# Kernel optimization log

Hardware: AMD Instinct MI355X
Metric: run time of the kernel (lower is better)

The kernel has to match this reference:

```python
import jax, jax.numpy as jnp
import numpy as np

N, D, H, DH, DFF, E = 4096, 512, 8, 64, 2048, 65536


def setup_inputs() -> dict:
    key = jax.random.key(0)
    ks = jax.random.split(key, 20)
    g = lambda k, s: jax.random.normal(k, s, dtype=jnp.float32) * 0.02
    inp = {
        'x': jax.random.normal(ks[0], (N, D), dtype=jnp.float32),
        'edge_index': jax.random.randint(ks[1], (2, E), 0, N),
        'edge_attr': jax.random.uniform(ks[2], (E,), dtype=jnp.float32),
        'Wg': g(ks[3], (D, D)), 'bg': jnp.zeros((D,), jnp.float32),
        'ln1_s': jnp.ones((D,), jnp.float32), 'ln1_b': jnp.zeros((D,), jnp.float32),
        'Wq': g(ks[4], (D, D)), 'bq': jnp.zeros((D,), jnp.float32),
        'Wk': g(ks[5], (D, D)), 'bk': jnp.zeros((D,), jnp.float32),
        'Wv': g(ks[6], (D, D)), 'bv': jnp.zeros((D,), jnp.float32),
        'Wo': g(ks[7], (D, D)), 'bo': jnp.zeros((D,), jnp.float32),
        'ln2_s': jnp.ones((D,), jnp.float32), 'ln2_b': jnp.zeros((D,), jnp.float32),
        'W1': g(ks[8], (D, DFF)), 'b1': jnp.zeros((DFF,), jnp.float32),
        'W2': g(ks[9], (DFF, D)), 'b2': jnp.zeros((D,), jnp.float32),
        'Wa': g(ks[10], (2 * D, D)), 'ba': jnp.zeros((D,), jnp.float32),
    }
    return inp


def _ln(x, s, b):
    m = x.mean(-1, keepdims=True)
    v = ((x - m) ** 2).mean(-1, keepdims=True)
    return (x - m) * jax.lax.rsqrt(v + 1e-5) * s + b


def _gcn(x, edge_index, ew, Wg, bg):
    # GCNConv: linear, add self-loops (weight 1), sym deg normalization, scatter-add
    xt = x @ Wg                                   # [N, D]
    src = jnp.concatenate([edge_index[0], jnp.arange(N)])
    dst = jnp.concatenate([edge_index[1], jnp.arange(N)])
    w = jnp.concatenate([ew, jnp.ones((N,), ew.dtype)])
    deg = jax.ops.segment_sum(w, dst, num_segments=N)
    dinv = jnp.where(deg > 0, jax.lax.rsqrt(jnp.maximum(deg, 1e-12)), 0.0)
    coef = dinv[src] * w * dinv[dst]              # [E+N]
    out = jax.ops.segment_sum(xt[src] * coef[:, None], dst, num_segments=N)
    return out + bg


def _tfm(x, p):
    # pre-LN vanilla transformer block over all N nodes as one sequence
    h = _ln(x, p['ln1_s'], p['ln1_b'])
    q = (h @ p['Wq'] + p['bq']).reshape(N, H, DH)
    k = (h @ p['Wk'] + p['bk']).reshape(N, H, DH)
    v = (h @ p['Wv'] + p['bv']).reshape(N, H, DH)
    scores = jnp.einsum('nhd,mhd->hnm', q, k) / np.sqrt(DH)
    a = jax.nn.softmax(scores, axis=-1)
    o = jnp.einsum('hnm,mhd->nhd', a, v).reshape(N, D)
    x = x + o @ p['Wo'] + p['bo']
    h2 = _ln(x, p['ln2_s'], p['ln2_b'])
    mlp = jax.nn.gelu(h2 @ p['W1'] + p['b1']) @ p['W2'] + p['b2']
    return x + mlp


def reference(x, edge_index, edge_attr, Wg, bg, ln1_s, ln1_b, Wq, bq, Wk, bk, Wv, bv,
              Wo, bo, ln2_s, ln2_b, W1, b1, W2, b2, Wa, ba):
    p = dict(ln1_s=ln1_s, ln1_b=ln1_b, Wq=Wq, bq=bq, Wk=Wk, bk=bk, Wv=Wv, bv=bv,
             Wo=Wo, bo=bo, ln2_s=ln2_s, ln2_b=ln2_b, W1=W1, b1=b1, W2=W2, b2=b2)
    mp = _gcn(x, edge_index, edge_attr, Wg, bg)
    tf = _tfm(x, p)
    return x + jnp.concatenate([mp, tf], axis=-1) @ Wa + ba
```

## Files before the change

### kernel.cpp

```cpp
#include <hip/hip_runtime.h>
#include <math.h>

#define N_NODES 4096
#define DMODEL  512
#define NHEAD   8
#define DHEAD   64
#define DFF     2048
#define NEDGE   65536
#define QKVLD   1536

typedef unsigned short u16;
typedef __bf16 bf16x8 __attribute__((ext_vector_type(8)));
typedef float  f32x4  __attribute__((ext_vector_type(4)));
typedef short  s16x4  __attribute__((ext_vector_type(4)));

#if defined(__has_builtin)
#if __has_builtin(__builtin_amdgcn_mfma_f32_16x16x16bf16_1k)
#define HAS_MFMA_1K 1
#endif
#endif

__device__ inline f32x4 mfma16(bf16x8 a, bf16x8 b, f32x4 c) {
    return __builtin_amdgcn_mfma_f32_16x16x32_bf16(a, b, c, 0, 0, 0);
}

#ifdef HAS_MFMA_1K
__device__ inline f32x4 mfma1k(s16x4 a, s16x4 b, f32x4 c) {
    return __builtin_amdgcn_mfma_f32_16x16x16bf16_1k(a, b, c, 0, 0, 0);
}
__device__ inline s16x4 pack_bf4(f32x4 p) {
    union { float f; unsigned u; } a0, a1, a2, a3;
    a0.f = p[0]; a1.f = p[1]; a2.f = p[2]; a3.f = p[3];
    unsigned lo = __builtin_amdgcn_perm(a1.u + 0x8000u, a0.u + 0x8000u, 0x07060302u);
    unsigned hi = __builtin_amdgcn_perm(a3.u + 0x8000u, a2.u + 0x8000u, 0x07060302u);
    union { unsigned u[2]; s16x4 v; } r;
    r.u[0] = lo; r.u[1] = hi;
    return r.v;
}
#endif

__device__ inline u16 f2bf(float f) {
    union { float f; unsigned u; } v; v.f = f;
    unsigned r = v.u + 0x7fff + ((v.u >> 16) & 1);
    return (u16)(r >> 16);
}

__device__ inline float bf2f(u16 v) {
    union { unsigned u; float f; } t; t.u = ((unsigned)v) << 16; return t.f;
}

__device__ inline float gelu_tanh(float x) {
    float x3 = x * x * x;
    float t = tanhf(0.7978845608028654f * (x + 0.044715f * x3));
    return 0.5f * x * (1.0f + t);
}

#define GBN 128
#define GBK 32
#define GP  40

template <int ACT, int OBF16>
__launch_bounds__(512)
__global__ void mfma_gemm64(const u16* __restrict__ A, const u16* __restrict__ Bt,
                            const float* __restrict__ bias, const float* __restrict__ res,
                            void* __restrict__ Cout, int M, int Nn, int K, float scale,
                            int ldC, int ldRes) {
    __shared__ u16 Asm[2][64 * GP];
    __shared__ u16 Bsm[2][128 * GP];

    const int tid = threadIdx.x;
    const int w = tid >> 6;
    const int lane = tid & 63;
    const int quad = lane >> 4;
    const int l15 = lane & 15;
    const int row0 = blockIdx.y * 64;
    const int col0 = blockIdx.x * GBN;
    const int rh = (w & 1) * 32;
    const int cg = (w >> 1) * 32;

    f32x4 acc[2][2];
#pragma unroll
    for (int i = 0; i < 2; ++i)
#pragma unroll
        for (int j = 0; j < 2; ++j) acc[i][j] = (f32x4){0.f, 0.f, 0.f, 0.f};

    const int brow = tid >> 2, bk = (tid & 3) * 8;
    const int arow = (tid & 255) >> 2, ak = (tid & 3) * 8;
    const bool doA = (tid < 256);

    {
        uint4 b0 = *(const uint4*)&Bt[(size_t)(col0 + brow) * K + bk];
        *(uint4*)&Bsm[0][brow * GP + bk] = b0;
        if (doA) {
            uint4 a0 = *(const uint4*)&A[(size_t)(row0 + arow) * K + ak];
            *(uint4*)&Asm[0][arow * GP + ak] = a0;
        }
    }
    __syncthreads();

    const int nT = K / GBK;
    for (int t = 0; t < nT; ++t) {
        const int buf = t & 1;
        uint4 an, bn;
        if (t + 1 < nT) {
            const int k0 = (t + 1) * GBK;
            bn = *(const uint4*)&Bt[(size_t)(col0 + brow) * K + k0 + bk];
            if (doA) an = *(const uint4*)&A[(size_t)(row0 + arow) * K + k0 + ak];
        }
        bf16x8 af[2], bf[2];
#pragma unroll
        for (int i = 0; i < 2; ++i)
            af[i] = *(const bf16x8*)&Asm[buf][(rh + i * 16 + l15) * GP + quad * 8];
#pragma unroll
        for (int j = 0; j < 2; ++j)
            bf[j] = *(const bf16x8*)&Bsm[buf][(cg + j * 16 + l15) * GP + quad * 8];
#pragma unroll
        for (int i = 0; i < 2; ++i)
#pragma unroll
            for (int j = 0; j < 2; ++j)
                acc[i][j] = mfma16(af[i], bf[j], acc[i][j]);
        if (t + 1 < nT) {
            *(uint4*)&Bsm[buf ^ 1][brow * GP + bk] = bn;
            if (doA) *(uint4*)&Asm[buf ^ 1][arow * GP + ak] = an;
            __syncthreads();
        }
    }

#pragma unroll
    for (int j = 0; j < 2; ++j) {
        const int col = col0 + cg + j * 16 + l15;
        const float bc = bias ? bias[col] : 0.f;
#pragma unroll
        for (int i = 0; i < 2; ++i) {
#pragma unroll
            for (int r = 0; r < 4; ++r) {
                const int row = row0 + rh + i * 16 + quad * 4 + r;
                float o = (acc[i][j][r] + bc) * scale;
                if (ACT == 1) o = gelu_tanh(o);
                if (res) o += res[(size_t)row * ldRes + col];
                if (OBF16)
                    ((u16*)Cout)[(size_t)row * ldC + col] = f2bf(o);
                else
                    ((float*)Cout)[(size_t)row * ldC + col] = o;
            }
        }
    }
}

__launch_bounds__(256)
__global__ void qkvg_gemm(const u16* __restrict__ xb, const u16* __restrict__ hb,
                          const u16* __restrict__ Wall,
                          const float* __restrict__ bq, const float* __restrict__ bk,
                          const float* __restrict__ bv,
                          u16* __restrict__ xtb, u16* __restrict__ qkvb,
                          u16* __restrict__ vtb) {
    __shared__ u16 Asm[2][64 * GP];
    __shared__ u16 Bsm[2][128 * GP];

    const int tid = threadIdx.x;
    const int w = tid >> 6;
    const int lane = tid & 63;
    const int quad = lane >> 4;
    const int l15 = lane & 15;
    const int row0 = blockIdx.y * 64;
    const int col0 = blockIdx.x * GBN;
    const int wn = w * 32;
    const int K = DMODEL;
    const u16* A = (col0 < 512) ? xb : hb;

    f32x4 acc[4][2];
#pragma unroll
    for (int i = 0; i < 4; ++i)
#pragma unroll
        for (int j = 0; j < 2; ++j) acc[i][j] = (f32x4){0.f, 0.f, 0.f, 0.f};

    const int c1 = tid, c2 = tid + 256;
    const int ar1 = c1 >> 2, ak1 = (c1 & 3) * 8;
    const int ar2 = c2 >> 2, ak2 = (c2 & 3) * 8;

    {
        uint4 a0 = *(const uint4*)&A   [(size_t)(row0 + ar1) * K + ak1];
        uint4 b0 = *(const uint4*)&Wall[(size_t)(col0 + ar1) * K + ak1];
        uint4 b1 = *(const uint4*)&Wall[(size_t)(col0 + ar2) * K + ak2];
        *(uint4*)&Asm[0][ar1 * GP + ak1] = a0;
        *(uint4*)&Bsm[0][ar1 * GP + ak1] = b0;
        *(uint4*)&Bsm[0][ar2 * GP + ak2] = b1;
    }
    __syncthreads();

    const int nT = K / GBK;
    for (int t = 0; t < nT; ++t) {
        const int buf = t & 1;
        uint4 an, bn0, bn1;
        if (t + 1 < nT) {
            const int k0 = (t + 1) * GBK;
            an  = *(const uint4*)&A   [(size_t)(row0 + ar1) * K + k0 + ak1];
            bn0 = *(const uint4*)&Wall[(size_t)(col0 + ar1) * K + k0 + ak1];
            bn1 = *(const uint4*)&Wall[(size_t)(col0 + ar2) * K + k0 + ak2];
        }
        bf16x8 af[4], bf[2];
#pragma unroll
        for (int i = 0; i < 4; ++i)
            af[i] = *(const bf16x8*)&Asm[buf][(i * 16 + l15) * GP + quad * 8];
#pragma unroll
        for (int j = 0; j < 2; ++j)
            bf[j] = *(const bf16x8*)&Bsm[buf][(wn + j * 16 + l15) * GP + quad * 8];
#pragma unroll
        for (int i = 0; i < 4; ++i)
#pragma unroll
            for (int j = 0; j < 2; ++j)
                acc[i][j] = mfma16(af[i], bf[j], acc[i][j]);
        if (t + 1 < nT) {
            *(uint4*)&Asm[buf ^ 1][ar1 * GP + ak1] = an;
            *(uint4*)&Bsm[buf ^ 1][ar1 * GP + ak1] = bn0;
            *(uint4*)&Bsm[buf ^ 1][ar2 * GP + ak2] = bn1;
            __syncthreads();
        }
    }

#pragma unroll
    for (int j = 0; j < 2; ++j) {
        const int col = col0 + wn + j * 16 + l15;
        if (col < 512) {
#pragma unroll
            for (int i = 0; i < 4; ++i)
#pragma unroll
                for (int r = 0; r < 4; ++r)
                    xtb[(size_t)(row0 + i * 16 + quad * 4 + r) * 512 + col] =
                        f2bf(acc[i][j][r]);
        } else if (col < 1536) {
            const float bc = (col < 1024) ? bq[col - 512] : bk[col - 1024];
            const float scale = (col < 1024) ? 0.125f : 1.0f;
#pragma unroll
            for (int i = 0; i < 4; ++i)
#pragma unroll
                for (int r = 0; r < 4; ++r)
                    qkvb[(size_t)(row0 + i * 16 + quad * 4 + r) * QKVLD + col - 512] =
                        f2bf((acc[i][j][r] + bc) * scale);
        } else {
            const int hd = col - 1536;
            const float bc = bv[hd];
#pragma unroll
            for (int i = 0; i < 4; ++i) {
                ushort4 pk;
                pk.x = f2bf(acc[i][j][0] + bc);
                pk.y = f2bf(acc[i][j][1] + bc);
                pk.z = f2bf(acc[i][j][2] + bc);
                pk.w = f2bf(acc[i][j][3] + bc);
                *(uint2*)&vtb[(size_t)hd * N_NODES + row0 + i * 16 + quad * 4] =
                    *(uint2*)&pk;
            }
        }
    }
}

__device__ inline float block_sum_256(float v, float* red4) {
#pragma unroll
    for (int o = 32; o > 0; o >>= 1) v += __shfl_down(v, o, 64);
    const int lane = threadIdx.x & 63;
    const int w = threadIdx.x >> 6;
    if (lane == 0) red4[w] = v;
    __syncthreads();
    return red4[0] + red4[1] + red4[2] + red4[3];
}

__launch_bounds__(256)
__global__ void prep_kernel(
    const float* __restrict__ Wg, const float* __restrict__ Wq,
    const float* __restrict__ Wk, const float* __restrict__ Wv,
    const float* __restrict__ Wo, const float* __restrict__ W1,
    const float* __restrict__ W2, const float* __restrict__ Wa,
    u16* __restrict__ Wgt, u16* __restrict__ Wqt, u16* __restrict__ Wkt,
    u16* __restrict__ Wvt, u16* __restrict__ Wot, u16* __restrict__ W1t,
    u16* __restrict__ W2t, u16* __restrict__ Wat,
    const float* __restrict__ x, u16* __restrict__ xb,
    const float* __restrict__ ln1s, const float* __restrict__ ln1b,
    u16* __restrict__ hb, float* __restrict__ deg, int* __restrict__ cnt) {
    __shared__ u16 t[32][34];
    __shared__ float redA[4];
    __shared__ float redB[4];
    const int id = blockIdx.x;

    if (id < 3840) {
        const float* W; u16* Wt; int K, Nn, bx, by;
        if (id < 1280) {
            const int m = id >> 8, tt = id & 255;
            bx = tt & 15; by = tt >> 4; K = 512; Nn = 512;
            W  = (m == 0) ? Wg  : (m == 1) ? Wq  : (m == 2) ? Wk  : (m == 3) ? Wv  : Wo;
            Wt = (m == 0) ? Wgt : (m == 1) ? Wqt : (m == 2) ? Wkt : (m == 3) ? Wvt : Wot;
        } else if (id < 2304) {
            const int tt = id - 1280; bx = tt & 63; by = tt >> 6;
            K = 512; Nn = 2048; W = W1; Wt = W1t;
        } else if (id < 3328) {
            const int tt = id - 2304; bx = tt & 15; by = tt >> 4;
            K = 2048; Nn = 512; W = W2; Wt = W2t;
        } else {
            const int tt = id - 3328; bx = tt & 15; by = tt >> 4;
            K = 1024; Nn = 512; W = Wa; Wt = Wat;
        }
        const int k0 = by * 32, n0 = bx * 32;
        const int r = threadIdx.x >> 3, c4 = (threadIdx.x & 7) * 4;
        float4 v = *(const float4*)&W[(size_t)(k0 + r) * Nn + n0 + c4];
        t[r][c4 + 0] = f2bf(v.x); t[r][c4 + 1] = f2bf(v.y);
        t[r][c4 + 2] = f2bf(v.z); t[r][c4 + 3] = f2bf(v.w);
        __syncthreads();
        u16 tmp[4];
#pragma unroll
        for (int i = 0; i < 4; ++i) tmp[i] = t[c4 + i][r];
        u16* op = Wt + (size_t)(n0 + r) * K + k0 + c4;
        *(uint2*)op = *(uint2*)tmp;
    } else if (id < 5888) {
        size_t i = ((size_t)(id - 3840) * 256 + threadIdx.x) * 4;
        float4 v = *(const float4*)&x[i];
        ushort4 o;
        o.x = f2bf(v.x); o.y = f2bf(v.y); o.z = f2bf(v.z); o.w = f2bf(v.w);
        *(ushort4*)&xb[i] = o;
    } else if (id < 9984) {
        const int row = id - 5888;
        const int tid = threadIdx.x;
        const float* xr = x + (size_t)row * DMODEL;
        float v0 = xr[tid], v1 = xr[tid + 256];
        float total = block_sum_256(v0 + v1, redA);
        float mean = total * (1.0f / DMODEL);
        float d0 = v0 - mean, d1 = v1 - mean;
        float sq = block_sum_256(d0 * d0 + d1 * d1, redB);
        float inv = rsqrtf(sq * (1.0f / DMODEL) + 1e-5f);
        hb[(size_t)row * DMODEL + tid] = f2bf(d0 * inv * ln1s[tid] + ln1b[tid]);
        hb[(size_t)row * DMODEL + tid + 256] =
            f2bf(d1 * inv * ln1s[tid + 256] + ln1b[tid + 256]);
    } else {
        int i = (id - 9984) * 256 + threadIdx.x;
        deg[i] = 1.0f;
        cnt[i] = 0;
    }
}

__launch_bounds__(256)
__global__ void ln_kernel(const float* __restrict__ X, const float* __restrict__ s,
                          const float* __restrict__ b, u16* __restrict__ Y) {
    __shared__ float redA[4];
    __shared__ float redB[4];
    const int row = blockIdx.x;
    const int tid = threadIdx.x;
    const float* xr = X + (size_t)row * DMODEL;
    float v0 = xr[tid], v1 = xr[tid + 256];
    float total = block_sum_256(v0 + v1, redA);
    float mean = total * (1.0f / DMODEL);
    float d0 = v0 - mean, d1 = v1 - mean;
    float sq = block_sum_256(d0 * d0 + d1 * d1, redB);
    float inv = rsqrtf(sq * (1.0f / DMODEL) + 1e-5f);
    Y[(size_t)row * DMODEL + tid] = f2bf(d0 * inv * s[tid] + b[tid]);
    Y[(size_t)row * DMODEL + tid + 256] = f2bf(d1 * inv * s[tid + 256] + b[tid + 256]);
}

__global__ void gcn_count_kernel(const int* __restrict__ ei, const float* __restrict__ ew,
                                 float* __restrict__ deg, int* __restrict__ cnt) {
    int e = blockIdx.x * 256 + threadIdx.x;
    int d = ei[NEDGE + e];
    atomicAdd(&cnt[d], 1);
    atomicAdd(&deg[d], ew[e]);
}

__launch_bounds__(256)
__global__ void gcn_prefix_kernel(const int* __restrict__ cnt, int* __restrict__ off,
                                  int* __restrict__ cur, const float* __restrict__ deg,
                                  float* __restrict__ dinv) {
    __shared__ int part[256];
    const int tid = threadIdx.x;
    int local[16];
    int s = 0;
#pragma unroll
    for (int i = 0; i < 16; ++i) { local[i] = s; s += cnt[tid * 16 + i]; }
    part[tid] = s;
#pragma unroll
    for (int i = 0; i < 16; ++i) {
        const int n = tid * 16 + i;
        float d = deg[n];
        dinv[n] = (d > 0.f) ? rsqrtf(fmaxf(d, 1e-12f)) : 0.f;
    }
    __syncthreads();
    if (tid == 0) {
        int run = 0;
        for (int j = 0; j < 256; ++j) { int t = part[j]; part[j] = run; run += t; }
        off[N_NODES] = run;
    }
    __syncthreads();
    int p = part[tid];
#pragma unroll
    for (int i = 0; i < 16; ++i) {
        off[tid * 16 + i] = p + local[i];
        cur[tid * 16 + i] = p + local[i];
    }
}

__global__ void gcn_fill_kernel(const int* __restrict__ ei, const float* __restrict__ ew,
                                int* __restrict__ cur, int* __restrict__ esrc,
                                float* __restrict__ eww) {
    int e = blockIdx.x * 256 + threadIdx.x;
    int s = ei[e], d = ei[NEDGE + e];
    int pos = atomicAdd(&cur[d], 1);
    esrc[pos] = s;
    eww[pos] = ew[e];
}

__launch_bounds__(256)
__global__ void gcn_gather_kernel(const u16* __restrict__ xtb, const int* __restrict__ off,
                                  const int* __restrict__ esrc, const float* __restrict__ eww,
                                  const float* __restrict__ dinv, const float* __restrict__ bg,
                                  u16* __restrict__ catb) {
    const int d = blockIdx.x;
    const int b0 = off[d], b1 = off[d + 1];
    const float did = dinv[d];
    const int c = threadIdx.x * 2;
    float a0 = 0.f, a1 = 0.f;
    for (int j = b0; j < b1; ++j) {
        const int s = esrc[j];
        const float coef = dinv[s] * eww[j] * did;
        const unsigned pv = *(const unsigned*)&xtb[(size_t)s * DMODEL + c];
        a0 += coef * bf2f((u16)(pv & 0xffff));
        a1 += coef * bf2f((u16)(pv >> 16));
    }
    {
        const unsigned pv = *(const unsigned*)&xtb[(size_t)d * DMODEL + c];
        const float sl = did * did;
        a0 += sl * bf2f((u16)(pv & 0xffff));
        a1 += sl * bf2f((u16)(pv >> 16));
    }
    const unsigned pk = (unsigned)f2bf(a0 + bg[c]) | ((unsigned)f2bf(a1 + bg[c + 1]) << 16);
    *(unsigned*)&catb[(size_t)d * 1024 + c] = pk;
}

#define TK 64
#define AP 72
#define NSPLIT 4
#define KSPAN (N_NODES / NSPLIT)

__launch_bounds__(256)
__global__ void attn_kernel(const u16* __restrict__ Qkv, const u16* __restrict__ Vtb,
                            float* __restrict__ Op0, float* __restrict__ Op1,
                            float* __restrict__ Op2, float* __restrict__ Op3,
                            float* __restrict__ lpart) {
    __shared__ u16 Ks[64 * AP];
    __shared__ u16 Vs[64 * AP];
#ifndef HAS_MFMA_1K
    __shared__ u16 Ps[4][2][16 * AP];
#endif

    const int h = blockIdx.x;
    const int q0 = blockIdx.y * 128;
    const int sp = blockIdx.z;
    float* __restrict__ Opx = (sp == 0) ? Op0 : (sp == 1) ? Op1 : (sp == 2) ? Op2 : Op3;
    const int kbase = sp * KSPAN;

    const int tid = threadIdx.x;
    const int w = tid >> 6;
    const int lane = tid & 63;
    const int quad = lane >> 4;
    const int l15 = lane & 15;

    const u16* qp = Qkv + (size_t)(q0 + w * 32 + l15) * QKVLD + h * DHEAD + quad * 8;
    bf16x8 qf[2][2];
    qf[0][0] = *(const bf16x8*)qp;
    qf[0][1] = *(const bf16x8*)(qp + 32);
    qf[1][0] = *(const bf16x8*)(qp + 16 * QKVLD);
    qf[1][1] = *(const bf16x8*)(qp + 16 * QKVLD + 32);

    f32x4 Oa[2][4];
#pragma unroll
    for (int a = 0; a < 2; ++a)
#pragma unroll
        for (int g = 0; g < 4; ++g) Oa[a][g] = (f32x4){0.f, 0.f, 0.f, 0.f};
    float ls[2] = {0.f, 0.f};

    const int srow = (tid & 127) >> 1;
    const int scol = (tid & 1) * 32;

    for (int kt = kbase; kt < kbase + KSPAN; kt += TK) {
        if (tid < 128) {
            const uint4* kg = (const uint4*)(Qkv + (size_t)(kt + srow) * QKVLD + 512 + h * DHEAD + scol);
            uint4* kd = (uint4*)&Ks[srow * AP + scol];
            kd[0] = kg[0]; kd[1] = kg[1]; kd[2] = kg[2]; kd[3] = kg[3];
        } else {
            const uint4* vg = (const uint4*)(Vtb + ((size_t)h * DHEAD + srow) * N_NODES + kt + scol);
            uint4* vd = (uint4*)&Vs[srow * AP + scol];
            vd[0] = vg[0]; vd[1] = vg[1]; vd[2] = vg[2]; vd[3] = vg[3];
        }
        __syncthreads();

        f32x4 St[2][4];
#pragma unroll
        for (int f = 0; f < 4; ++f) {
            const u16* kr = &Ks[(f * 16 + l15) * AP + quad * 8];
            bf16x8 k0 = *(const bf16x8*)kr;
            bf16x8 k1 = *(const bf16x8*)(kr + 32);
#pragma unroll
            for (int a = 0; a < 2; ++a) {
                f32x4 z = (f32x4){0.f, 0.f, 0.f, 0.f};
                z = mfma16(k0, qf[a][0], z);
                St[a][f] = mfma16(k1, qf[a][1], z);
            }
        }

#ifdef HAS_MFMA_1K
        s16x4 pk[2][4];
#pragma unroll
        for (int a = 0; a < 2; ++a)
#pragma unroll
            for (int f = 0; f < 4; ++f) {
                f32x4 p;
                p[0] = __expf(St[a][f][0]);
                p[1] = __expf(St[a][f][1]);
                p[2] = __expf(St[a][f][2]);
                p[3] = __expf(St[a][f][3]);
                ls[a] += (p[0] + p[1]) + (p[2] + p[3]);
                pk[a][f] = pack_bf4(p);
            }
#pragma unroll
        for (int f = 0; f < 4; ++f)
#pragma unroll
            for (int g = 0; g < 4; ++g) {
                const s16x4 vv = *(const s16x4*)&Vs[(g * 16 + l15) * AP + f * 16 + quad * 4];
                Oa[0][g] = mfma1k(pk[0][f], vv, Oa[0][g]);
                Oa[1][g] = mfma1k(pk[1][f], vv, Oa[1][g]);
            }
#else
        bf16x8 pa[2][2];
#pragma unroll
        for (int a = 0; a < 2; ++a) {
            u16* pw = Ps[w][a];
#pragma unroll
            for (int f = 0; f < 4; ++f) {
                float p0 = __expf(St[a][f][0]);
                float p1 = __expf(St[a][f][1]);
                float p2 = __expf(St[a][f][2]);
                float p3 = __expf(St[a][f][3]);
                ls[a] += (p0 + p1) + (p2 + p3);
                ushort4 pkk;
                pkk.x = f2bf(p0); pkk.y = f2bf(p1); pkk.z = f2bf(p2); pkk.w = f2bf(p3);
                *(uint2*)&pw[l15 * AP + f * 16 + quad * 4] = *(uint2*)&pkk;
            }
            const u16* pr = &pw[l15 * AP + quad * 8];
            pa[a][0] = *(const bf16x8*)pr;
            pa[a][1] = *(const bf16x8*)(pr + 32);
        }
#pragma unroll
        for (int g = 0; g < 4; ++g) {
            const u16* vr = &Vs[(g * 16 + l15) * AP + quad * 8];
            bf16x8 v0 = *(const bf16x8*)vr;
            bf16x8 v1 = *(const bf16x8*)(vr + 32);
#pragma unroll
            for (int a = 0; a < 2; ++a) {
                Oa[a][g] = mfma16(pa[a][0], v0, Oa[a][g]);
                Oa[a][g] = mfma16(pa[a][1], v1, Oa[a][g]);
            }
        }
#endif
        __syncthreads();
    }

#pragma unroll
    for (int a = 0; a < 2; ++a) {
        float s = ls[a];
        s += __shfl_xor(s, 16, 64);
        s += __shfl_xor(s, 32, 64);
        const int rowbase = q0 + w * 32 + a * 16;
        if (quad == 0)
            lpart[(size_t)(sp * NHEAD + h) * N_NODES + rowbase + l15] = s;
#pragma unroll
        for (int r = 0; r < 4; ++r) {
            float* op = Opx + (size_t)(rowbase + quad * 4 + r) * DMODEL + h * DHEAD + l15;
#pragma unroll
            for (int g = 0; g < 4; ++g) op[g * 16] = Oa[a][g][r];
        }
    }
}

__global__ void attn_reduce_kernel(const float* __restrict__ Op0, const float* __restrict__ Op1,
                                   const float* __restrict__ Op2, const float* __restrict__ Op3,
                                   const float* __restrict__ lpart, u16* __restrict__ attb) {
    size_t i4 = ((size_t)blockIdx.x * 256 + threadIdx.x) * 4;
    const int row = (int)(i4 >> 9);
    const int h = ((int)i4 & 511) >> 6;
    float4 o0 = *(const float4*)&Op0[i4];
    float4 o1 = *(const float4*)&Op1[i4];
    float4 o2 = *(const float4*)&Op2[i4];
    float4 o3 = *(const float4*)&Op3[i4];
    const float* lp = lpart + (size_t)h * N_NODES + row;
    const size_t S = (size_t)NHEAD * N_NODES;
    float inv = 1.0f / (lp[0] + lp[S] + lp[2 * S] + lp[3 * S]);
    ushort4 r;
    r.x = f2bf((o0.x + o1.x + o2.x + o3.x) * inv);
    r.y = f2bf((o0.y + o1.y + o2.y + o3.y) * inv);
    r.z = f2bf((o0.z + o1.z + o2.z + o3.z) * inv);
    r.w = f2bf((o0.w + o1.w + o2.w + o3.w) * inv);
    *(ushort4*)&attb[i4] = r;
}

static void mgemm64(hipStream_t st, const u16* A, const u16* Bt, const float* bias,
                    const float* res, void* C, int M, int Nn, int K, float scale,
                    int act, int obf16, int ldC, int ldRes) {
    dim3 g(Nn / GBN, M / 64), b(512);
    if (act)
        hipLaunchKernelGGL((mfma_gemm64<1, 1>), g, b, 0, st, A, Bt, bias, res, C, M, Nn, K, scale, ldC, ldRes);
    else if (obf16)
        hipLaunchKernelGGL((mfma_gemm64<0, 1>), g, b, 0, st, A, Bt, bias, res, C, M, Nn, K, scale, ldC, ldRes);
    else
        hipLaunchKernelGGL((mfma_gemm64<0, 0>), g, b, 0, st, A, Bt, bias, res, C, M, Nn, K, scale, ldC, ldRes);
}

extern "C" void kernel_launch(void* const* d_in, const int* in_sizes, int n_in,
                              void* d_out, int out_size, void* d_ws, size_t ws_size,
                              hipStream_t stream) {
    const float* x    = (const float*)d_in[0];
    const int*   ei   = (const int*)d_in[1];
    const float* ew   = (const float*)d_in[2];
    const float* Wg   = (const float*)d_in[3];
    const float* bg   = (const float*)d_in[4];
    const float* ln1s = (const float*)d_in[5];
    const float* ln1b = (const float*)d_in[6];
    const float* Wq   = (const float*)d_in[7];
    const float* bq   = (const float*)d_in[8];
    const float* Wk   = (const float*)d_in[9];
    const float* bk   = (const float*)d_in[10];
    const float* Wv   = (const float*)d_in[11];
    const float* bv   = (const float*)d_in[12];
    const float* Wo   = (const float*)d_in[13];
    const float* bo   = (const float*)d_in[14];
    const float* ln2s = (const float*)d_in[15];
    const float* ln2b = (const float*)d_in[16];
    const float* W1   = (const float*)d_in[17];
    const float* b1   = (const float*)d_in[18];
    const float* W2   = (const float*)d_in[19];
    const float* b2   = (const float*)d_in[20];
    const float* Wa   = (const float*)d_in[21];
    const float* ba   = (const float*)d_in[22];
    float* out = (float*)d_out;
    float* ws  = (float*)d_ws;

    const size_t SLOT = (size_t)N_NODES * DMODEL;

    u16*   xtb = (u16*)ws;
    float* Op2 = ws;
    float* x1  = ws;
    float* lpart = ws + SLOT;
    int*   esrc  = (int*)(ws + SLOT + 262144);
    float* eww   = (float*)(esrc + NEDGE);
    int*   off   = (int*)(eww + NEDGE);
    int*   cur   = off + 4100;
    int*   cnt   = cur + 4096;
    float* Op3 = ws + 2 * SLOT;
    u16* hb   = (u16*)(ws + 3 * SLOT);
    u16* attb = hb + SLOT;
    u16* h2b  = hb + SLOT;
    u16* qkvb = (u16*)(ws + 4 * SLOT);
    u16* vtb  = (u16*)(ws + 5 * SLOT) + SLOT;
    float* Op0  = ws + 6 * SLOT;
    float* Op1  = ws + 7 * SLOT;
    u16*   midb = (u16*)(ws + 6 * SLOT);
    u16* catb = (u16*)(ws + 8 * SLOT);
    u16* xb   = catb;
    u16* Wgt = (u16*)(ws + 9 * SLOT);
    u16* Wqt = Wgt + 262144;
    u16* Wkt = Wqt + 262144;
    u16* Wvt = Wkt + 262144;
    u16* Wot = Wvt + 262144;
    u16* W1t = Wot + 262144;
    u16* W2t = W1t + 1048576;
    u16* Wat = W2t + 1048576;
    float* deg  = (float*)(Wat + 524288);
    float* dinv = deg + N_NODES;

    hipLaunchKernelGGL(prep_kernel, dim3(10000), dim3(256), 0, stream,
                       Wg, Wq, Wk, Wv, Wo, W1, W2, Wa,
                       Wgt, Wqt, Wkt, Wvt, Wot, W1t, W2t, Wat,
                       x, xb, ln1s, ln1b, hb, deg, cnt);

    hipLaunchKernelGGL(qkvg_gemm, dim3(16, 64), dim3(256), 0, stream,
                       xb, hb, Wgt, bq, bk, bv, xtb, qkvb, vtb);

    hipLaunchKernelGGL(gcn_count_kernel, dim3(NEDGE / 256), dim3(256), 0, stream, ei, ew, deg, cnt);
    hipLaunchKernelGGL(gcn_prefix_kernel, dim3(1), dim3(256), 0, stream, cnt, off, cur, deg, dinv);
    hipLaunchKernelGGL(gcn_fill_kernel, dim3(NEDGE / 256), dim3(256), 0, stream, ei, ew, cur, esrc, eww);
    hipLaunchKernelGGL(gcn_gather_kernel, dim3(N_NODES), dim3(256), 0, stream,
                       xtb, off, esrc, eww, dinv, bg, catb);

    hipLaunchKernelGGL(attn_kernel, dim3(NHEAD, N_NODES / 128, NSPLIT), dim3(256), 0, stream,
                       qkvb, vtb, Op0, Op1, Op2, Op3, lpart);
    hipLaunchKernelGGL(attn_reduce_kernel, dim3((int)(SLOT / 1024)), dim3(256), 0, stream,
                       Op0, Op1, Op2, Op3, lpart, attb);

    mgemm64(stream, attb, Wot, bo, x, x1, N_NODES, DMODEL, DMODEL, 1.0f, 0, 0, DMODEL, DMODEL);
    hipLaunchKernelGGL(ln_kernel, dim3(N_NODES), dim3(256), 0, stream, x1, ln2s, ln2b, h2b);
    mgemm64(stream, h2b, W1t, b1, nullptr, midb, N_NODES, DFF, DMODEL, 1.0f, 1, 1, DFF, DFF);
    mgemm64(stream, midb, W2t, b2, x1, catb + 512, N_NODES, DMODEL, DFF, 1.0f, 0, 1, 1024, DMODEL);

    mgemm64(stream, catb, Wat, ba, x, out, N_NODES, DMODEL, 2 * DMODEL, 1.0f, 0, 0, DMODEL, DMODEL);
}
```

Before: 340.7 us.

## Double attention key splits, store bf16 partials, fold log2e into Q scale

Raises the attention key-split count from 4 to 8 to launch more blocks, and stores the per-split partial outputs in bf16 instead of fp32, packing two splits per workspace slot. The Q scale now includes log2(e), so the softmax uses the hardware exp2 instruction instead of __expf. The reduce kernel sums eight bf16 partials and eight row-sum entries, and the lpart region and esrc offset are enlarged to fit. This trades lower partial-output precision and an extra reduction pass over more data for more parallelism and less partial-output memory traffic.

```diff
diff --git a/kernel.cpp b/kernel.cpp
--- a/kernel.cpp
+++ b/kernel.cpp
@@ -19,6 +19,10 @@
 #define HAS_MFMA_1K 1
 #endif
 #endif
+
+__device__ inline float fast_exp2(float x) {
+    return __builtin_amdgcn_exp2f(x);
+}
 
 __device__ inline f32x4 mfma16(bf16x8 a, bf16x8 b, f32x4 c) {
     return __builtin_amdgcn_mfma_f32_16x16x32_bf16(a, b, c, 0, 0, 0);
@@ -147,6 +151,8 @@
     }
 }
 
+#define QSCALE 0.1803368801111204f
+
 __launch_bounds__(256)
 __global__ void qkvg_gemm(const u16* __restrict__ xb, const u16* __restrict__ hb,
                           const u16* __restrict__ Wall,
@@ -230,7 +236,7 @@
                         f2bf(acc[i][j][r]);
         } else if (col < 1536) {
             const float bc = (col < 1024) ? bq[col - 512] : bk[col - 1024];
-            const float scale = (col < 1024) ? 0.125f : 1.0f;
+            const float scale = (col < 1024) ? QSCALE : 1.0f;
 #pragma unroll
             for (int i = 0; i < 4; ++i)
 #pragma unroll
@@ -432,13 +438,13 @@
 
 #define TK 64
 #define AP 72
-#define NSPLIT 4
+#define NSPLIT 8
 #define KSPAN (N_NODES / NSPLIT)
 
 __launch_bounds__(256)
 __global__ void attn_kernel(const u16* __restrict__ Qkv, const u16* __restrict__ Vtb,
-                            float* __restrict__ Op0, float* __restrict__ Op1,
-                            float* __restrict__ Op2, float* __restrict__ Op3,
+                            u16* __restrict__ Ob0, u16* __restrict__ Ob1,
+                            u16* __restrict__ Ob2, u16* __restrict__ Ob3,
                             float* __restrict__ lpart) {
     __shared__ u16 Ks[64 * AP];
     __shared__ u16 Vs[64 * AP];
@@ -449,7 +455,8 @@
     const int h = blockIdx.x;
     const int q0 = blockIdx.y * 128;
     const int sp = blockIdx.z;
-    float* __restrict__ Opx = (sp == 0) ? Op0 : (sp == 1) ? Op1 : (sp == 2) ? Op2 : Op3;
+    u16* bases0 = (sp < 2) ? Ob0 : (sp < 4) ? Ob1 : (sp < 6) ? Ob2 : Ob3;
+    u16* __restrict__ Opx = bases0 + (size_t)(sp & 1) * N_NODES * DMODEL;
     const int kbase = sp * KSPAN;
 
     const int tid = threadIdx.x;
@@ -508,10 +515,10 @@
 #pragma unroll
             for (int f = 0; f < 4; ++f) {
                 f32x4 p;
-                p[0] = __expf(St[a][f][0]);
-                p[1] = __expf(St[a][f][1]);
-                p[2] = __expf(St[a][f][2]);
-                p[3] = __expf(St[a][f][3]);
+                p[0] = fast_exp2(St[a][f][0]);
+                p[1] = fast_exp2(St[a][f][1]);
+                p[2] = fast_exp2(St[a][f][2]);
+                p[3] = fast_exp2(St[a][f][3]);
                 ls[a] += (p[0] + p[1]) + (p[2] + p[3]);
                 pk[a][f] = pack_bf4(p);
             }
@@ -530,10 +537,10 @@
             u16* pw = Ps[w][a];
 #pragma unroll
             for (int f = 0; f < 4; ++f) {
-                float p0 = __expf(St[a][f][0]);
-                float p1 = __expf(St[a][f][1]);
-                float p2 = __expf(St[a][f][2]);
-                float p3 = __expf(St[a][f][3]);
+                float p0 = fast_exp2(St[a][f][0]);
+                float p1 = fast_exp2(St[a][f][1]);
+                float p2 = fast_exp2(St[a][f][2]);
+                float p3 = fast_exp2(St[a][f][3]);
                 ls[a] += (p0 + p1) + (p2 + p3);
                 ushort4 pkk;
                 pkk.x = f2bf(p0); pkk.y = f2bf(p1); pkk.z = f2bf(p2); pkk.w = f2bf(p3);
@@ -568,31 +575,39 @@
             lpart[(size_t)(sp * NHEAD + h) * N_NODES + rowbase + l15] = s;
 #pragma unroll
         for (int r = 0; r < 4; ++r) {
-            float* op = Opx + (size_t)(rowbase + quad * 4 + r) * DMODEL + h * DHEAD + l15;
-#pragma unroll
-            for (int g = 0; g < 4; ++g) op[g * 16] = Oa[a][g][r];
-        }
-    }
-}
-
-__global__ void attn_reduce_kernel(const float* __restrict__ Op0, const float* __restrict__ Op1,
-                                   const float* __restrict__ Op2, const float* __restrict__ Op3,
+            u16* op = Opx + (size_t)(rowbase + quad * 4 + r) * DMODEL + h * DHEAD + l15;
+#pragma unroll
+            for (int g = 0; g < 4; ++g) op[g * 16] = f2bf(Oa[a][g][r]);
+        }
+    }
+}
+
+__global__ void attn_reduce_kernel(const u16* __restrict__ Ob0, const u16* __restrict__ Ob1,
+                                   const u16* __restrict__ Ob2, const u16* __restrict__ Ob3,
                                    const float* __restrict__ lpart, u16* __restrict__ attb) {
     size_t i4 = ((size_t)blockIdx.x * 256 + threadIdx.x) * 4;
     const int row = (int)(i4 >> 9);
     const int h = ((int)i4 & 511) >> 6;
-    float4 o0 = *(const float4*)&Op0[i4];
-    float4 o1 = *(const float4*)&Op1[i4];
-    float4 o2 = *(const float4*)&Op2[i4];
-    float4 o3 = *(const float4*)&Op3[i4];
+    const size_t OFF = (size_t)N_NODES * DMODEL;
+    const u16* bases[4] = {Ob0, Ob1, Ob2, Ob3};
+    float s0 = 0.f, s1 = 0.f, s2 = 0.f, s3 = 0.f;
+#pragma unroll
+    for (int b = 0; b < 4; ++b)
+#pragma unroll
+        for (int k = 0; k < 2; ++k) {
+            uint2 v = *(const uint2*)(bases[b] + k * OFF + i4);
+            s0 += bf2f((u16)(v.x & 0xffff)); s1 += bf2f((u16)(v.x >> 16));
+            s2 += bf2f((u16)(v.y & 0xffff)); s3 += bf2f((u16)(v.y >> 16));
+        }
     const float* lp = lpart + (size_t)h * N_NODES + row;
     const size_t S = (size_t)NHEAD * N_NODES;
-    float inv = 1.0f / (lp[0] + lp[S] + lp[2 * S] + lp[3 * S]);
+    float l = 0.f;
+#pragma unroll
+    for (int sp = 0; sp < NSPLIT; ++sp) l += lp[sp * S];
+    const float inv = 1.0f / l;
     ushort4 r;
-    r.x = f2bf((o0.x + o1.x + o2.x + o3.x) * inv);
-    r.y = f2bf((o0.y + o1.y + o2.y + o3.y) * inv);
-    r.z = f2bf((o0.z + o1.z + o2.z + o3.z) * inv);
-    r.w = f2bf((o0.w + o1.w + o2.w + o3.w) * inv);
+    r.x = f2bf(s0 * inv); r.y = f2bf(s1 * inv);
+    r.z = f2bf(s2 * inv); r.w = f2bf(s3 * inv);
     *(ushort4*)&attb[i4] = r;
 }
 
@@ -640,23 +655,23 @@
     const size_t SLOT = (size_t)N_NODES * DMODEL;
 
     u16*   xtb = (u16*)ws;
-    float* Op2 = ws;
+    u16*   Ob0 = (u16*)ws;
     float* x1  = ws;
     float* lpart = ws + SLOT;
-    int*   esrc  = (int*)(ws + SLOT + 262144);
+    int*   esrc  = (int*)(ws + SLOT + 327680);
     float* eww   = (float*)(esrc + NEDGE);
     int*   off   = (int*)(eww + NEDGE);
     int*   cur   = off + 4100;
     int*   cnt   = cur + 4096;
-    float* Op3 = ws + 2 * SLOT;
+    u16* Ob1 = (u16*)(ws + 2 * SLOT);
     u16* hb   = (u16*)(ws + 3 * SLOT);
     u16* attb = hb + SLOT;
     u16* h2b  = hb + SLOT;
     u16* qkvb = (u16*)(ws + 4 * SLOT);
     u16* vtb  = (u16*)(ws + 5 * SLOT) + SLOT;
-    float* Op0  = ws + 6 * SLOT;
-    float* Op1  = ws + 7 * SLOT;
-    u16*   midb = (u16*)(ws + 6 * SLOT);
+    u16* Ob2  = (u16*)(ws + 6 * SLOT);
+    u16* Ob3  = (u16*)(ws + 7 * SLOT);
+    u16* midb = (u16*)(ws + 6 * SLOT);
     u16* catb = (u16*)(ws + 8 * SLOT);
     u16* xb   = catb;
     u16* Wgt = (u16*)(ws + 9 * SLOT);
@@ -685,9 +700,9 @@
                        xtb, off, esrc, eww, dinv, bg, catb);
 
     hipLaunchKernelGGL(attn_kernel, dim3(NHEAD, N_NODES / 128, NSPLIT), dim3(256), 0, stream,
-                       qkvb, vtb, Op0, Op1, Op2, Op3, lpart);
+                       qkvb, vtb, Ob0, Ob1, Ob2, Ob3, lpart);
     hipLaunchKernelGGL(attn_reduce_kernel, dim3((int)(SLOT / 1024)), dim3(256), 0, stream,
-                       Op0, Op1, Op2, Op3, lpart, attb);
+                       Ob0, Ob1, Ob2, Ob3, lpart, attb);
 
     mgemm64(stream, attb, Wot, bo, x, x1, N_NODES, DMODEL, DMODEL, 1.0f, 0, 0, DMODEL, DMODEL);
     hipLaunchKernelGGL(ln_kernel, dim3(N_NODES), dim3(256), 0, stream, x1, ln2s, ln2b, h2b);
```

After: 340.6 us. About the same (-0.0%).
